# Optimization experiments

Measured on AMD Instinct MI355X. Metric: run time of the kernel, lower is better.

## Reference

```python
import jax, jax.numpy as jnp
import numpy as np

B, E, F, Q = 8, 2000, 6000, 20
D = 256   # entity_dim == word_dim (required: word_embedding output feeds LSTM with input_size=word_dim)
WD = 256
L = 3
NUM_ENTITY, NUM_REL, NUM_WORD = 400000, 6000, 60000
NNZ = 2 * B * F
PAGERANK_LAMBDA, FACT_SCALE = 0.8, 3.0
VERY_NEG = -100000000000.0
VERY_SMALL = 1e-10


def _lin(x, W, b):
    return x @ W.T + b


def _sparse_bmm(indices, values, x, num_rows):
    # indices: [3, nnz] = (batch, row, col); x: [B, C, Dx] -> out [B, num_rows, Dx]
    b, r, c = indices[0], indices[1], indices[2]
    contrib = values[:, None] * x[b, c]
    seg = b * num_rows + r
    out = jax.ops.segment_sum(contrib, seg, num_segments=x.shape[0] * num_rows)
    return out.reshape(x.shape[0], num_rows, x.shape[2])


def _lstm(x, Wih, Whh, bih, bhh):
    # PyTorch LSTM, batch_first, 1 layer, unidirectional; gate order i,f,g,o
    Bb, T, _ = x.shape
    H = Whh.shape[1]
    def step(carry, xt):
        h, c = carry
        g = xt @ Wih.T + bih + h @ Whh.T + bhh
        i, f, gg, o = jnp.split(g, 4, axis=-1)
        c = jax.nn.sigmoid(f) * c + jax.nn.sigmoid(i) * jnp.tanh(gg)
        h = jax.nn.sigmoid(o) * jnp.tanh(c)
        return (h, c), h
    init = (jnp.zeros((Bb, H), x.dtype), jnp.zeros((Bb, H), x.dtype))
    (h, c), hs = jax.lax.scan(step, init, jnp.swapaxes(x, 0, 1))
    return jnp.swapaxes(hs, 0, 1), h


def setup_inputs():
    key = jax.random.key(0)
    ks = iter(jax.random.split(key, 48))
    p = lambda shape: jax.random.normal(next(ks), shape, jnp.float32) * 0.02
    inp = {}
    inp['local_entity'] = jax.random.randint(next(ks), (B, E), 0, NUM_ENTITY + 1)
    inp['q2e_adj_mat'] = (jax.random.uniform(next(ks), (B, E, 1)) < 0.01).astype(jnp.float32)
    inp['kb_fact_rel'] = jax.random.randint(next(ks), (B, F), 0, NUM_REL)
    inp['query_text'] = jax.random.randint(next(ks), (B, Q), 0, NUM_WORD)
    inp['answer_dist'] = (jax.random.uniform(next(ks), (B, E)) < 0.005).astype(jnp.float32)
    eb = jax.random.randint(next(ks), (NNZ,), 0, B)
    ef = jax.random.randint(next(ks), (NNZ,), 0, F)
    ee = jax.random.randint(next(ks), (NNZ,), 0, E)
    inp['e2f_indices'] = jnp.stack([eb, ef, ee])
    inp['e2f_val'] = jnp.ones((NNZ,), jnp.float32)
    fb = jax.random.randint(next(ks), (NNZ,), 0, B)
    fe = jax.random.randint(next(ks), (NNZ,), 0, E)
    ff = jax.random.randint(next(ks), (NNZ,), 0, F)
    inp['f2e_indices'] = jnp.stack([fb, fe, ff])
    inp['f2e_val'] = jnp.ones((NNZ,), jnp.float32)
    inp['entity_table'] = p((NUM_ENTITY + 1, WD)).at[-1].set(0.0)
    inp['ent_lin_W'] = p((D, WD)); inp['ent_lin_b'] = jnp.zeros((D,), jnp.float32)
    inp['relation_table'] = p((NUM_REL + 1, WD)).at[-1].set(0.0)
    inp['rel_lin_W'] = p((D, WD)); inp['rel_lin_b'] = jnp.zeros((D,), jnp.float32)
    inp['word_table'] = p((NUM_WORD + 1, D)).at[-1].set(0.0)
    inp['lstm_Wih'] = p((4 * D, WD)); inp['lstm_Whh'] = p((4 * D, D))
    inp['lstm_bih'] = jnp.zeros((4 * D,), jnp.float32); inp['lstm_bhh'] = jnp.zeros((4 * D,), jnp.float32)
    inp['q2e_W'] = p((L, D, D)); inp['q2e_b'] = jnp.zeros((L, D), jnp.float32)
    inp['e2q_W'] = p((L, D, 3 * D)); inp['e2q_b'] = jnp.zeros((L, D), jnp.float32)
    inp['e2e_W'] = p((L, D, 3 * D)); inp['e2e_b'] = jnp.zeros((L, D), jnp.float32)
    inp['head_W'] = p((L, D, D)); inp['head_b'] = jnp.zeros((L, D), jnp.float32)
    inp['tail_W'] = p((L, D, D)); inp['tail_b'] = jnp.zeros((L, D), jnp.float32)
    inp['self_W'] = p((L, D, D)); inp['self_b'] = jnp.zeros((L, D), jnp.float32)
    inp['score_W'] = p((1, D)); inp['score_b'] = jnp.zeros((1,), jnp.float32)
    return inp


def reference(local_entity, q2e_adj_mat, kb_fact_rel, query_text, answer_dist, e2f_indices, e2f_val, f2e_indices, f2e_val, entity_table, ent_lin_W, ent_lin_b, relation_table, rel_lin_W, rel_lin_b, word_table, lstm_Wih, lstm_Whh, lstm_bih, lstm_bhh, q2e_W, q2e_b, e2q_W, e2q_b, e2e_W, e2e_b, head_W, head_b, tail_W, tail_b, self_W, self_b, score_W, score_b):
    query_mask = (query_text != NUM_WORD).astype(jnp.float32)          # [B,Q]
    local_entity_mask = (local_entity != NUM_ENTITY).astype(jnp.float32)
    # query encoder (dropout = identity in eval)
    query_hidden, h_last = _lstm(word_table[query_text], lstm_Wih, lstm_Whh, lstm_bih, lstm_bhh)
    query_node_emb = h_last[:, None, :]                                # [B,1,D]
    local_fact_emb = _lin(relation_table[kb_fact_rel], rel_lin_W, rel_lin_b)  # [B,F,D]
    div = jnp.sqrt(jnp.float32(D))
    sim = jnp.einsum('bqd,bfd->bqf', query_hidden, local_fact_emb) / div
    sim = jax.nn.softmax(sim + (1.0 - query_mask)[:, :, None] * VERY_NEG, axis=1)
    att = jnp.einsum('bqf,bqd->bfd', sim, query_hidden)
    Wt = jnp.sum(att * local_fact_emb, axis=2) / div                   # [B,F]
    W_tilde = jnp.exp(Wt - jnp.max(Wt, axis=1, keepdims=True))
    e2fT = jnp.stack([e2f_indices[0], e2f_indices[2], e2f_indices[1]])  # transpose(1,2)
    e2f_softmax = _sparse_bmm(e2fT, e2f_val, W_tilde[:, :, None], E)[..., 0]
    e2f_softmax = jnp.maximum(e2f_softmax, VERY_SMALL)
    pagerank_f = q2e_adj_mat[..., 0]                                    # [B,E]
    local_entity_emb = _lin(entity_table[local_entity], ent_lin_W, ent_lin_b)  # [B,E,D]
    for i in range(L):
        q2e_emb = jnp.broadcast_to(_lin(query_node_emb, q2e_W[i], q2e_b[i]), (B, E, D))
        nxt = jnp.concatenate([local_entity_emb, q2e_emb], axis=2)
        e2f_emb = jax.nn.relu(_lin(local_fact_emb, self_W[i], self_b[i]) + _sparse_bmm(e2f_indices, e2f_val, _lin(local_entity_emb, head_W[i], head_b[i]), F))
        e2f_norm = W_tilde[:, :, None] * _sparse_bmm(e2f_indices, e2f_val, (pagerank_f / e2f_softmax)[:, :, None], F)
        e2f_emb = e2f_emb * e2f_norm
        f2e_emb = jax.nn.relu(_lin(local_entity_emb, self_W[i], self_b[i]) + _sparse_bmm(f2e_indices, f2e_val, _lin(e2f_emb, tail_W[i], tail_b[i]), E))
        pagerank_f = PAGERANK_LAMBDA * _sparse_bmm(f2e_indices, f2e_val, e2f_norm, E)[..., 0] + (1.0 - PAGERANK_LAMBDA) * pagerank_f
        nxt = jnp.concatenate([nxt, FACT_SCALE * f2e_emb], axis=2)      # [B,E,3D]
        query_node_emb = jnp.einsum('be,bed->bd', pagerank_f, _lin(nxt, e2q_W[i], e2q_b[i]))[:, None, :]
        local_entity_emb = jax.nn.relu(_lin(nxt, e2e_W[i], e2e_b[i]))
    score = _lin(local_entity_emb, score_W, score_b)[..., 0]            # [B,E]
    loss = jnp.mean(jnp.maximum(score, 0.0) - score * answer_dist + jnp.log1p(jnp.exp(-jnp.abs(score))))
    score_m = score + (1.0 - local_entity_mask) * VERY_NEG
    pred = jnp.argmax(score_m, axis=1)
    pred_dist = jax.nn.sigmoid(score_m) * local_entity_mask
    return (loss, pred, pred_dist)
```

## Files before the change

### kernel.cpp

```cpp
#include <hip/hip_runtime.h>
#include <math.h>

#define BB 8
#define EE 2000
#define FF 6000
#define QQ 20
#define DD 256
#define NENT 400000
#define NWORD 60000
#define NNZ_ 96000
#define VNEG  (-1e11f)
#define VSMALL 1e-10f

typedef __attribute__((ext_vector_type(8))) short short8v;
typedef __attribute__((ext_vector_type(4))) short short4v;
typedef __attribute__((ext_vector_type(4))) float f32x4;

__device__ __forceinline__ unsigned short f2bf_rne(float x)
{
    unsigned u = __float_as_uint(x);
    u += 0x7FFFu + ((u >> 16) & 1u);
    return (unsigned short)(u >> 16);
}
__device__ __forceinline__ float bf2f(unsigned short h)
{
    return __uint_as_float((unsigned)h << 16);
}

template<int GATHER, int DUALW, int RELU, int RS, int BIASB>
__device__ __forceinline__ void mgemm_body(
    const float* __restrict__ A1, const int* __restrict__ idx,
    const float* __restrict__ A2, float sA2,
    const short* __restrict__ W1h, const short* __restrict__ W1l,
    const short* __restrict__ W2h, const short* __restrict__ W2l,
    const float* __restrict__ biasA,
    const float* __restrict__ rowscale, const float* __restrict__ bias2,
    float* __restrict__ out, int by, int bx,
    short* __restrict__ Ah, short* __restrict__ Al)
{
    const int tid = threadIdx.x;
    const int lane = tid & 63, wv = tid >> 6;
    const int wrow = wv >> 1, wcol = wv & 1;
    const int row0 = by * 128, col0 = bx * 128;

    const int sr = tid >> 1;
    const int sko = (tid & 1) << 5;
    const int grow = row0 + sr;
    const float* aRow1 = GATHER ? A1 + (size_t)idx[grow] * 256 : A1 + (size_t)grow * 256;
    const float* aRow2 = DUALW ? A2 + (size_t)grow * 256 : nullptr;

    f32x4 acc[4][4];
    #pragma unroll
    for (int i = 0; i < 4; ++i)
        #pragma unroll
        for (int j = 0; j < 4; ++j) acc[i][j] = (f32x4){0.f, 0.f, 0.f, 0.f};

    const int nch = DUALW ? 8 : 4;
    for (int ch = 0; ch < nch; ++ch) {
        const bool hi2 = DUALW && (ch >= 4);
        const float* ar = hi2 ? aRow2 : aRow1;
        const int kbase = (ch & 3) << 6;
        #pragma unroll
        for (int q = 0; q < 8; ++q) {
            const int kc = sko + (q << 2);
            float4 a = *(const float4*)(ar + kbase + kc);
            if (DUALW && hi2) { a.x *= sA2; a.y *= sA2; a.z *= sA2; a.w *= sA2; }
            unsigned short h0 = f2bf_rne(a.x), h1 = f2bf_rne(a.y),
                           h2 = f2bf_rne(a.z), h3 = f2bf_rne(a.w);
            unsigned short l0 = f2bf_rne(a.x - bf2f(h0)), l1 = f2bf_rne(a.y - bf2f(h1)),
                           l2 = f2bf_rne(a.z - bf2f(h2)), l3 = f2bf_rne(a.w - bf2f(h3));
            const int tI = ((sr >> 4) << 1) + (kc >> 5);
            const int off = (tI << 9) + ((((sr & 15)) + (((kc >> 3) & 3) << 4)) << 3) + (kc & 7);
            *(short4v*)(Ah + off) = (short4v){(short)h0, (short)h1, (short)h2, (short)h3};
            *(short4v*)(Al + off) = (short4v){(short)l0, (short)l1, (short)l2, (short)l3};
        }
        __syncthreads();
        const short* Wh = hi2 ? W2h : W1h;
        const short* Wl = hi2 ? W2l : W1l;
        #pragma unroll
        for (int ks = 0; ks < 2; ++ks) {
            const int kg = kbase + (ks << 5) + ((lane >> 4) << 3);
            short8v bh[4], bl[4];
            #pragma unroll
            for (int ct = 0; ct < 4; ++ct) {
                const int c = col0 + (wcol << 6) + (ct << 4) + (lane & 15);
                bh[ct] = *(const short8v*)(Wh + (size_t)c * 256 + kg);
                bl[ct] = *(const short8v*)(Wl + (size_t)c * 256 + kg);
            }
            #pragma unroll
            for (int rt = 0; rt < 4; ++rt) {
                const int tI = (((wrow << 2) + rt) << 1) + ks;
                const short8v avh = *(const short8v*)(Ah + (tI << 9) + (lane << 3));
                const short8v avl = *(const short8v*)(Al + (tI << 9) + (lane << 3));
                #pragma unroll
                for (int ct = 0; ct < 4; ++ct) {
                    acc[rt][ct] = __builtin_amdgcn_mfma_f32_16x16x32_bf16(avh, bh[ct], acc[rt][ct], 0, 0, 0);
                    acc[rt][ct] = __builtin_amdgcn_mfma_f32_16x16x32_bf16(avh, bl[ct], acc[rt][ct], 0, 0, 0);
                    acc[rt][ct] = __builtin_amdgcn_mfma_f32_16x16x32_bf16(avl, bh[ct], acc[rt][ct], 0, 0, 0);
                }
            }
        }
        __syncthreads();
    }
    #pragma unroll
    for (int rt = 0; rt < 4; ++rt) {
        const int rb = row0 + (wrow << 6) + (rt << 4) + ((lane >> 4) << 2);
        #pragma unroll
        for (int ct = 0; ct < 4; ++ct) {
            const int c = col0 + (wcol << 6) + (ct << 4) + (lane & 15);
            #pragma unroll
            for (int j = 0; j < 4; ++j) {
                const int r = rb + j;
                float v = acc[rt][ct][j];
                v += BIASB ? biasA[(size_t)(r / EE) * 256 + c] : biasA[c];
                if (RS) v += rowscale[r] * bias2[c];
                if (RELU) v = fmaxf(v, 0.f);
                out[(size_t)r * 256 + c] = v;
            }
        }
    }
}

template<int GATHER, int DUALW, int RELU, int RS, int BIASB>
__global__ __launch_bounds__(256, 2) void mgemm_k(
    const float* __restrict__ A1, const int* __restrict__ idx,
    const float* __restrict__ A2, float sA2,
    const short* __restrict__ W1h, const short* __restrict__ W1l,
    const short* __restrict__ W2h, const short* __restrict__ W2l,
    const float* __restrict__ biasA,
    const float* __restrict__ rowscale, const float* __restrict__ bias2,
    float* __restrict__ out)
{
    __shared__ short Ah[16 * 512];
    __shared__ short Al[16 * 512];
    mgemm_body<GATHER, DUALW, RELU, RS, BIASB>(A1, idx, A2, sA2, W1h, W1l, W2h, W2l,
        biasA, rowscale, bias2, out, blockIdx.y, blockIdx.x, Ah, Al);
}

template<int GATHER>
__global__ __launch_bounds__(256, 2) void mgemm_pair_k(
    const float* __restrict__ Aa, const int* __restrict__ idxA,
    const short* __restrict__ Wah, const short* __restrict__ Wal,
    const float* __restrict__ ba, float* __restrict__ outa, int nya,
    const float* __restrict__ Ab, const int* __restrict__ idxB,
    const short* __restrict__ Wbh, const short* __restrict__ Wbl,
    const float* __restrict__ bb, float* __restrict__ outb)
{
    __shared__ short Ah[16 * 512];
    __shared__ short Al[16 * 512];
    const int by = blockIdx.y;
    if (by < nya)
        mgemm_body<GATHER, 0, 0, 0, 0>(Aa, idxA, nullptr, 1.f, Wah, Wal, nullptr, nullptr,
            ba, nullptr, nullptr, outa, by, blockIdx.x, Ah, Al);
    else
        mgemm_body<GATHER, 0, 0, 0, 0>(Ab, idxB, nullptr, 1.f, Wbh, Wbl, nullptr, nullptr,
            bb, nullptr, nullptr, outb, by - nya, blockIdx.x, Ah, Al);
}

__global__ void wpack_k(const float* __restrict__ relW, const float* __restrict__ entW,
                        const float* __restrict__ headW, const float* __restrict__ tailW,
                        const float* __restrict__ selfW, const float* __restrict__ e2eW,
                        short* __restrict__ wh, short* __restrict__ wl)
{
    int id = blockIdx.x * 256 + threadIdx.x;
    if (id >= 17 * 65536) return;
    int m = id >> 16, e = id & 65535;
    float x;
    if (m == 0)       x = relW[e];
    else if (m == 1)  x = entW[e];
    else if (m < 5)   x = headW[(size_t)(m - 2) * 65536 + e];
    else if (m < 8)   x = tailW[(size_t)(m - 5) * 65536 + e];
    else if (m < 11)  x = selfW[(size_t)(m - 8) * 65536 + e];
    else if (m < 14)  x = e2eW[(size_t)(m - 11) * 196608 + (size_t)(e >> 8) * 768 + (e & 255)];
    else              x = e2eW[(size_t)(m - 14) * 196608 + (size_t)(e >> 8) * 768 + 512 + (e & 255)];
    unsigned short h = f2bf_rne(x);
    wh[id] = (short)h;
    wl[id] = (short)f2bf_rne(x - bf2f(h));
}

template<int GATHER>
__global__ __launch_bounds__(256, 4) void gemm3_k(
    const float* __restrict__ A1, const int* __restrict__ idx,
    const float* __restrict__ W1, int ldw1,
    const float* __restrict__ biasA,
    float* __restrict__ out, int M, int N)
{
    __shared__ float As[16][68];
    __shared__ float Bs[16][132];
    const int tid = threadIdx.x;
    const int row0 = blockIdx.y * 64, col0 = blockIdx.x * 128;
    const int tx = tid & 15, ty = tid >> 4;
    const int srA = tid >> 2, skA = (tid & 3) << 2;
    const int srB = tid >> 1, skB = (tid & 1) << 3;
    const int grA = row0 + srA;
    const bool rvalid = (grA < M);
    const float* aRow1 = nullptr;
    if (rvalid) aRow1 = GATHER ? A1 + (size_t)idx[grA] * 256 : A1 + (size_t)grA * 256;
    const float* wR1 = W1 + (size_t)(col0 + srB) * ldw1;

    float acc[4][8];
    #pragma unroll
    for (int i = 0; i < 4; ++i)
        #pragma unroll
        for (int j = 0; j < 8; ++j) acc[i][j] = 0.f;

    float4 a0, b0, b1;
    auto fetch = [&](int ch) {
        const int k0 = ch << 4;
        if (rvalid) a0 = *(const float4*)(aRow1 + k0 + skA);
        else        a0 = make_float4(0.f, 0.f, 0.f, 0.f);
        b0 = *(const float4*)(wR1 + k0 + skB);
        b1 = *(const float4*)(wR1 + k0 + skB + 4);
    };

    fetch(0);
    for (int ch = 0; ch < 16; ++ch) {
        As[skA + 0][srA] = a0.x; As[skA + 1][srA] = a0.y;
        As[skA + 2][srA] = a0.z; As[skA + 3][srA] = a0.w;
        Bs[skB + 0][srB] = b0.x; Bs[skB + 1][srB] = b0.y;
        Bs[skB + 2][srB] = b0.z; Bs[skB + 3][srB] = b0.w;
        Bs[skB + 4][srB] = b1.x; Bs[skB + 5][srB] = b1.y;
        Bs[skB + 6][srB] = b1.z; Bs[skB + 7][srB] = b1.w;
        __syncthreads();
        if (ch + 1 < 16) fetch(ch + 1);
        #pragma unroll
        for (int kk = 0; kk < 16; ++kk) {
            float av[4], bv[8];
            *(float4*)&av[0] = *(const float4*)&As[kk][ty << 2];
            *(float4*)&bv[0] = *(const float4*)&Bs[kk][tx << 2];
            *(float4*)&bv[4] = *(const float4*)&Bs[kk][(tx << 2) + 64];
            #pragma unroll
            for (int i = 0; i < 4; ++i)
                #pragma unroll
                for (int j = 0; j < 8; ++j) acc[i][j] += av[i] * bv[j];
        }
        __syncthreads();
    }
    #pragma unroll
    for (int i = 0; i < 4; ++i) {
        int r = row0 + (ty << 2) + i;
        if (r >= M) continue;
        float* orow = out + (size_t)r * N;
        #pragma unroll
        for (int jh = 0; jh < 2; ++jh) {
            const int c = col0 + (jh << 6) + (tx << 2);
            float4 v;
            v.x = acc[i][jh * 4 + 0] + biasA[c + 0];
            v.y = acc[i][jh * 4 + 1] + biasA[c + 1];
            v.z = acc[i][jh * 4 + 2] + biasA[c + 2];
            v.w = acc[i][jh * 4 + 3] + biasA[c + 3];
            *(float4*)(orow + c) = v;
        }
    }
}

__global__ void csr_count2_k(const int* __restrict__ idxA, int* __restrict__ cntA,
                             const int* __restrict__ idxB, int* __restrict__ cntB)
{
    int k = blockIdx.x * 256 + threadIdx.x;
    if (k >= NNZ_) return;
    if (blockIdx.y == 0) atomicAdd(&cntA[idxA[k] * FF + idxA[NNZ_ + k]], 1);
    else                 atomicAdd(&cntB[idxB[k] * EE + idxB[NNZ_ + k]], 1);
}

__global__ __launch_bounds__(1024) void scan2_k(
    const int* __restrict__ cntA, int* __restrict__ rpA, int* __restrict__ curA, int nA,
    const int* __restrict__ cntB, int* __restrict__ rpB, int* __restrict__ curB, int nB)
{
    const int* cnt = blockIdx.x ? cntB : cntA;
    int* rp  = blockIdx.x ? rpB  : rpA;
    int* cur = blockIdx.x ? curB : curA;
    int n    = blockIdx.x ? nB   : nA;
    __shared__ int sums[1024];
    int t = threadIdx.x;
    int chunk = (n + 1023) / 1024;
    int lo = t * chunk, hi = lo + chunk;
    if (lo > n) lo = n;
    if (hi > n) hi = n;
    int s = 0;
    for (int i = lo; i < hi; ++i) s += cnt[i];
    sums[t] = s;
    __syncthreads();
    for (int off = 1; off < 1024; off <<= 1) {
        int v = (t >= off) ? sums[t - off] : 0;
        __syncthreads();
        sums[t] += v;
        __syncthreads();
    }
    int run = (t == 0) ? 0 : sums[t - 1];
    for (int i = lo; i < hi; ++i) { rp[i] = run; cur[i] = run; run += cnt[i]; }
    if (hi == n) rp[n] = run;
}

__global__ void csr_fill2_k(
    const int* __restrict__ idxA, const float* __restrict__ valA,
    int* __restrict__ curA, int* __restrict__ colA, float* __restrict__ vpA,
    const int* __restrict__ idxB, const float* __restrict__ valB,
    int* __restrict__ curB, int* __restrict__ colB, float* __restrict__ vpB)
{
    int k = blockIdx.x * 256 + threadIdx.x;
    if (k >= NNZ_) return;
    if (blockIdx.y == 0) {
        int row = idxA[k] * FF + idxA[NNZ_ + k];
        int p = atomicAdd(&curA[row], 1);
        colA[p] = idxA[2 * NNZ_ + k];
        vpA[p] = valA[k];
    } else {
        int row = idxB[k] * EE + idxB[NNZ_ + k];
        int p = atomicAdd(&curB[row], 1);
        colB[p] = idxB[2 * NNZ_ + k];
        vpB[p] = valB[k];
    }
}

__global__ void degw_k(const int* __restrict__ rp, const float* __restrict__ vp,
                       float* __restrict__ degw, int n)
{
    int r = blockIdx.x * 256 + threadIdx.x;
    if (r >= n) return;
    float s = 0.f;
    for (int j = rp[r]; j < rp[r + 1]; ++j) s += vp[j];
    degw[r] = s;
}

__global__ __launch_bounds__(256) void gather_fused_e2f_k(
    const int* __restrict__ rowptr, const int* __restrict__ col,
    const float* __restrict__ valp, const float* __restrict__ headsrc,
    const float* __restrict__ pr, const float* __restrict__ sm,
    const float* __restrict__ Wtil, float* __restrict__ e2fnrm,
    float* __restrict__ dst, int nrows)
{
    int gid = blockIdx.x * 256 + threadIdx.x;
    int row = gid >> 6, lane = gid & 63;
    if (row >= nrows) return;
    int b = row / FF;
    const float* prb = pr + (size_t)b * EE;
    const float* smb = sm + (size_t)b * EE;
    float4* dp = (float4*)(dst + (size_t)row * DD + (lane << 2));
    float4 acc = *dp;
    float ns = 0.f;
    int j0 = rowptr[row], j1 = rowptr[row + 1];
    for (int j = j0; j < j1; ++j) {
        int c = col[j];
        float v = valp[j];
        float4 x = *(const float4*)(headsrc + ((size_t)b * EE + c) * DD + (lane << 2));
        acc.x += v * x.x; acc.y += v * x.y; acc.z += v * x.z; acc.w += v * x.w;
        ns += v * (prb[c] / fmaxf(smb[c], VSMALL));
    }
    float nrm = Wtil[row] * ns;
    if (lane == 0) e2fnrm[row] = nrm;
    acc.x = fmaxf(acc.x, 0.f) * nrm; acc.y = fmaxf(acc.y, 0.f) * nrm;
    acc.z = fmaxf(acc.z, 0.f) * nrm; acc.w = fmaxf(acc.w, 0.f) * nrm;
    *dp = acc;
}

__global__ __launch_bounds__(256) void gather_sum_k(
    const int* __restrict__ rowptr, const int* __restrict__ col,
    const float* __restrict__ valp, const float* __restrict__ src,
    float* __restrict__ dst, int nrows, int nrPerB, int ncs)
{
    int gid = blockIdx.x * 256 + threadIdx.x;
    int row = gid >> 6, lane = gid & 63;
    if (row >= nrows) return;
    int b = row / nrPerB;
    float4 acc = make_float4(0.f, 0.f, 0.f, 0.f);
    int j0 = rowptr[row], j1 = rowptr[row + 1];
    for (int j = j0; j < j1; ++j) {
        int c = col[j];
        float v = valp[j];
        float4 x = *(const float4*)(src + ((size_t)b * ncs + c) * DD + (lane << 2));
        acc.x += v * x.x; acc.y += v * x.y; acc.z += v * x.z; acc.w += v * x.w;
    }
    *(float4*)(dst + (size_t)row * DD + (lane << 2)) = acc;
}

#define LSTM_BLOCKS 64
__global__ __launch_bounds__(256, 1) void lstm2_k(
    const float* __restrict__ Xg, const float* __restrict__ Whh,
    const float* __restrict__ bhh, float* __restrict__ gbuf,
    unsigned* __restrict__ bar, float* __restrict__ qh, float* __restrict__ qne)
{
    __shared__ float wslice[128 * 257];
    __shared__ float hbuf[256];
    __shared__ float cbuf[256];
    __shared__ float gpart[256];
    const int B = blockIdx.x;
    const int b = B >> 3, p = B & 7;
    const int t = threadIdx.x;
    const float* wsrc = Whh + (size_t)p * 128 * 256;
    for (int i = t; i < 128 * 64; i += 256) {
        int row = i >> 6, q4 = (i & 63) << 2;
        float4 w = *(const float4*)(wsrc + (size_t)row * 256 + q4);
        float* d = &wslice[row * 257 + q4];
        d[0] = w.x; d[1] = w.y; d[2] = w.z; d[3] = w.w;
    }
    hbuf[t] = 0.f; cbuf[t] = 0.f;
    __syncthreads();

    unsigned* bar_cnt = bar;
    unsigned* bar_gen = bar + 1;

    for (int step = 0; step < QQ; ++step) {
        {
            const int r = t & 127, half = t >> 7;
            const float* wr = &wslice[r * 257 + half * 128];
            const float* hb = &hbuf[half * 128];
            float acc = 0.f;
            #pragma unroll 8
            for (int k = 0; k < 128; ++k) acc += wr[k] * hb[k];
            gpart[t] = acc;
        }
        __syncthreads();
        if (t < 128) {
            const int gr = p * 128 + t;
            float g = bhh[gr] + Xg[((size_t)b * QQ + step) * 1024 + gr]
                    + gpart[t] + gpart[t + 128];
            gbuf[((size_t)(step & 1) * BB + b) * 1024 + gr] = g;
        }
        __syncthreads();
        if (t == 0) {
            __threadfence();
            const unsigned target = (unsigned)(step + 1) * LSTM_BLOCKS;
            unsigned old = atomicAdd(bar_cnt, 1u);
            if (old == target - 1u) {
                atomicExch(bar_gen, (unsigned)(step + 1));
            } else {
                while (atomicAdd(bar_gen, 0u) < (unsigned)(step + 1)) {}
            }
            __threadfence();
        }
        __syncthreads();
        {
            const float* g = gbuf + ((size_t)(step & 1) * BB + b) * 1024;
            float gi = g[t], gf = g[256 + t], gg = g[512 + t], go = g[768 + t];
            float si = 1.f / (1.f + expf(-gi));
            float sf = 1.f / (1.f + expf(-gf));
            float so = 1.f / (1.f + expf(-go));
            float c = sf * cbuf[t] + si * tanhf(gg);
            float hh = so * tanhf(c);
            cbuf[t] = c;
            hbuf[t] = hh;
            if (p == 0) qh[((size_t)b * QQ + step) * DD + t] = hh;
        }
        __syncthreads();
    }
    if (p == 0) qne[(size_t)b * DD + t] = hbuf[t];
}

__global__ __launch_bounds__(256) void simwt_k(
    const float* __restrict__ qhid, const int* __restrict__ qtext,
    const float* __restrict__ lfe, float* __restrict__ Wt)
{
    __shared__ float qs[QQ * DD];
    __shared__ float qmn[QQ];
    const int b = blockIdx.y;
    const int f = blockIdx.x * 256 + threadIdx.x;
    for (int i = threadIdx.x; i < QQ * DD; i += 256) qs[i] = qhid[(size_t)b * QQ * DD + i];
    if (threadIdx.x < QQ)
        qmn[threadIdx.x] = (qtext[b * QQ + threadIdx.x] != NWORD) ? 0.f : VNEG;
    __syncthreads();
    if (f >= FF) return;
    float acc[QQ];
    #pragma unroll
    for (int q = 0; q < QQ; ++q) acc[q] = 0.f;
    const float* lr = lfe + ((size_t)b * FF + f) * DD;
    for (int d = 0; d < DD; d += 4) {
        float4 x = *(const float4*)(lr + d);
        #pragma unroll
        for (int q = 0; q < QQ; ++q) {
            float4 y = *(const float4*)&qs[q * DD + d];
            acc[q] += x.x * y.x + x.y * y.y + x.z * y.z + x.w * y.w;
        }
    }
    const float inv = 0.0625f;
    float pre[QQ], m = -INFINITY;
    #pragma unroll
    for (int q = 0; q < QQ; ++q) { pre[q] = acc[q] * inv + qmn[q]; m = fmaxf(m, pre[q]); }
    float s = 0.f;
    #pragma unroll
    for (int q = 0; q < QQ; ++q) s += expf(pre[q] - m);
    float wt = 0.f;
    #pragma unroll
    for (int q = 0; q < QQ; ++q) wt += (expf(pre[q] - m) / s) * (acc[q] * inv);
    Wt[(size_t)b * FF + f] = wt;
}

__global__ __launch_bounds__(256) void rowmax_wtil_k(
    const float* __restrict__ Wt, float* __restrict__ Wtil)
{
    __shared__ float red[256];
    int b = blockIdx.x, t = threadIdx.x;
    float m = -INFINITY;
    for (int f = t; f < FF; f += 256) m = fmaxf(m, Wt[b * FF + f]);
    red[t] = m; __syncthreads();
    for (int s = 128; s > 0; s >>= 1) {
        if (t < s) red[t] = fmaxf(red[t], red[t + s]);
        __syncthreads();
    }
    float mx = red[0];
    for (int f = t; f < FF; f += 256) Wtil[b * FF + f] = expf(Wt[b * FF + f] - mx);
}

__global__ void scatter_sm_k(const int* __restrict__ idx, const float* __restrict__ val,
                             const float* __restrict__ Wtil, float* __restrict__ dst)
{
    int k = blockIdx.x * 256 + threadIdx.x;
    if (k >= NNZ_) return;
    int b = idx[k], e = idx[2 * NNZ_ + k], f = idx[NNZ_ + k];
    atomicAdd(&dst[(size_t)b * EE + e], val[k] * Wtil[(size_t)b * FF + f]);
}

__global__ __launch_bounds__(256) void qlin_ebias_k(
    const float* __restrict__ qne, const float* __restrict__ q2eW,
    const float* __restrict__ q2eb, const float* __restrict__ e2eW,
    const float* __restrict__ e2eb, float* __restrict__ qlin, float* __restrict__ ebias)
{
    __shared__ float xs[DD], qs[DD];
    int b = blockIdx.x, j = threadIdx.x;
    xs[j] = qne[b * DD + j];
    __syncthreads();
    float acc = q2eb[j];
    const float* wr = q2eW + (size_t)j * DD;
    #pragma unroll 4
    for (int k = 0; k < DD; k += 4) {
        float4 w = *(const float4*)(wr + k);
        acc += xs[k] * w.x + xs[k + 1] * w.y + xs[k + 2] * w.z + xs[k + 3] * w.w;
    }
    qlin[b * DD + j] = acc;
    qs[j] = acc;
    __syncthreads();
    float acc2 = e2eb[j];
    const float* wr2 = e2eW + (size_t)j * 768 + 256;
    #pragma unroll 4
    for (int k = 0; k < DD; k += 4) {
        float4 w = *(const float4*)(wr2 + k);
        acc2 += qs[k] * w.x + qs[k + 1] * w.y + qs[k + 2] * w.z + qs[k + 3] * w.w;
    }
    ebias[b * DD + j] = acc2;
}

#define VCH 80
#define NCHK (EE / VCH)
__global__ __launch_bounds__(256) void vreduce_pr_k(
    const int* __restrict__ f2e_rp, const int* __restrict__ f2e_col,
    const float* __restrict__ f2e_vp, const float* __restrict__ e2fnrm,
    float* __restrict__ pr, const float* __restrict__ lee,
    const float* __restrict__ f2e, float* __restrict__ vpartL,
    float* __restrict__ vpartF, float* __restrict__ vpartS)
{
    int b = blockIdx.y, ch = blockIdx.x, k = threadIdx.x;
    int e0 = ch * VCH;
    __shared__ float prs[VCH];
    if (k < VCH) {
        int row = b * EE + e0 + k;
        float s = 0.f;
        for (int j = f2e_rp[row]; j < f2e_rp[row + 1]; ++j)
            s += f2e_vp[j] * e2fnrm[(size_t)b * FF + f2e_col[j]];
        float v = 0.8f * s + 0.2f * pr[row];
        pr[row] = v;
        prs[k] = v;
    }
    __syncthreads();
    float a1 = 0.f, a2 = 0.f;
    for (int e = 0; e < VCH; ++e) {
        float p = prs[e];
        size_t base = ((size_t)b * EE + e0 + e) * DD + k;
        a1 += p * lee[base];
        a2 += p * f2e[base];
    }
    int pi = ch * BB + b;
    vpartL[(size_t)pi * DD + k] = a1;
    vpartF[(size_t)pi * DD + k] = a2;
    float sp = 0.f;
    for (int e = k; e < VCH; e += 256) sp += prs[e];
    __shared__ float red[256];
    red[k] = sp; __syncthreads();
    for (int s = 128; s > 0; s >>= 1) {
        if (k < s) red[k] += red[k + s];
        __syncthreads();
    }
    if (k == 0) vpartS[pi] = red[0];
}

__global__ __launch_bounds__(256) void qneupd_qlin_k(
    const float* __restrict__ vpartL, const float* __restrict__ vpartF,
    const float* __restrict__ vpartS, const float* __restrict__ qlinCur,
    const float* __restrict__ W, const float* __restrict__ bias,
    float* __restrict__ qne,
    const float* __restrict__ q2eWn, const float* __restrict__ q2ebn,
    const float* __restrict__ e2eWn, const float* __restrict__ e2ebn,
    float* __restrict__ qlinNext, float* __restrict__ ebiasNext)
{
    __shared__ float s1[DD], s2[DD], s3[DD], qn[DD], qs[DD];
    int b = blockIdx.x, j = threadIdx.x;
    float a1 = 0.f, a3 = 0.f, sp = 0.f;
    for (int ch = 0; ch < NCHK; ++ch) {
        int pi = ch * BB + b;
        a1 += vpartL[(size_t)pi * DD + j];
        a3 += vpartF[(size_t)pi * DD + j];
        sp += vpartS[pi];
    }
    s1[j] = a1; s2[j] = qlinCur[b * DD + j]; s3[j] = a3;
    __syncthreads();
    float acc = sp * bias[j];
    const float* wr = W + (size_t)j * 768;
    #pragma unroll 4
    for (int k = 0; k < DD; k += 4) {
        float4 w0 = *(const float4*)(wr + k);
        float4 w1 = *(const float4*)(wr + 256 + k);
        float4 w2 = *(const float4*)(wr + 512 + k);
        acc += s1[k] * w0.x + s1[k + 1] * w0.y + s1[k + 2] * w0.z + s1[k + 3] * w0.w;
        acc += sp * (s2[k] * w1.x + s2[k + 1] * w1.y + s2[k + 2] * w1.z + s2[k + 3] * w1.w);
        acc += 3.f * (s3[k] * w2.x + s3[k + 1] * w2.y + s3[k + 2] * w2.z + s3[k + 3] * w2.w);
    }
    qne[b * DD + j] = acc;
    qn[j] = acc;
    __syncthreads();
    float aq = q2ebn[j];
    const float* wq = q2eWn + (size_t)j * DD;
    #pragma unroll 4
    for (int k = 0; k < DD; k += 4) {
        float4 w = *(const float4*)(wq + k);
        aq += qn[k] * w.x + qn[k + 1] * w.y + qn[k + 2] * w.z + qn[k + 3] * w.w;
    }
    qlinNext[b * DD + j] = aq;
    qs[j] = aq;
    __syncthreads();
    float ae = e2ebn[j];
    const float* we = e2eWn + (size_t)j * 768 + 256;
    #pragma unroll 4
    for (int k = 0; k < DD; k += 4) {
        float4 w = *(const float4*)(we + k);
        ae += qs[k] * w.x + qs[k + 1] * w.y + qs[k + 2] * w.z + qs[k + 3] * w.w;
    }
    ebiasNext[b * DD + j] = ae;
}

__global__ __launch_bounds__(256) void final_part_k(
    const float* __restrict__ lee, const float* __restrict__ sw_,
    const float* __restrict__ sb, const int* __restrict__ local_entity,
    const float* __restrict__ ans, float* __restrict__ out,
    float* __restrict__ fpl, float* __restrict__ fpv, int* __restrict__ fpi)
{
    __shared__ float sw[DD];
    int b = blockIdx.x >> 3, ch = blockIdx.x & 7, t = threadIdx.x;
    sw[t] = sw_[t];
    __syncthreads();
    float sb0 = sb[0];
    float lsum = 0.f, bm = -INFINITY;
    int bi = EE;
    int e0 = ch * 250;
    for (int e = e0 + t; e < e0 + 250; e += 256) {
        const float* a = lee + ((size_t)b * EE + e) * DD;
        float s = sb0;
        for (int k = 0; k < DD; k += 4) {
            float4 v = *(const float4*)(a + k);
            s += v.x * sw[k] + v.y * sw[k + 1] + v.z * sw[k + 2] + v.w * sw[k + 3];
        }
        float mask = (local_entity[b * EE + e] != NENT) ? 1.f : 0.f;
        float smv = s + (1.f - mask) * VNEG;
        float sig;
        if (smv >= 0.f) sig = 1.f / (1.f + expf(-smv));
        else { float es = expf(smv); sig = es / (1.f + es); }
        out[1 + BB + b * EE + e] = sig * mask;
        lsum += fmaxf(s, 0.f) - s * ans[b * EE + e] + log1pf(expf(-fabsf(s)));
        if (smv > bm) { bm = smv; bi = e; }
    }
    __shared__ float rv[256]; __shared__ int ri[256]; __shared__ float rl[256];
    rv[t] = bm; ri[t] = bi; rl[t] = lsum;
    __syncthreads();
    for (int s = 128; s > 0; s >>= 1) {
        if (t < s) {
            rl[t] += rl[t + s];
            if (rv[t + s] > rv[t] || (rv[t + s] == rv[t] && ri[t + s] < ri[t])) {
                rv[t] = rv[t + s]; ri[t] = ri[t + s];
            }
        }
        __syncthreads();
    }
    if (t == 0) { fpl[blockIdx.x] = rl[0]; fpv[blockIdx.x] = rv[0]; fpi[blockIdx.x] = ri[0]; }
}

__global__ void final_combine_k(const float* __restrict__ fpl,
                                const float* __restrict__ fpv,
                                const int* __restrict__ fpi, float* __restrict__ out)
{
    __shared__ float lsums[BB];
    int t = threadIdx.x;
    if (t < BB) {
        float ls = 0.f, bm = -INFINITY;
        int bi = EE;
        for (int ch = 0; ch < 8; ++ch) {
            int i = t * 8 + ch;
            ls += fpl[i];
            if (fpv[i] > bm || (fpv[i] == bm && fpi[i] < bi)) { bm = fpv[i]; bi = fpi[i]; }
        }
        out[1 + t] = (float)bi;
        lsums[t] = ls;
    }
    __syncthreads();
    if (t == 0) {
        float s = 0.f;
        for (int b = 0; b < BB; ++b) s += lsums[b];
        out[0] = s / (float)(BB * EE);
    }
}

extern "C" void kernel_launch(void* const* d_in, const int* in_sizes, int n_in,
                              void* d_out, int out_size, void* d_ws, size_t ws_size,
                              hipStream_t stream)
{
    (void)in_sizes; (void)n_in; (void)out_size; (void)ws_size;
    const int*   local_entity = (const int*)d_in[0];
    const float* q2e_adj      = (const float*)d_in[1];
    const int*   kb_fact_rel  = (const int*)d_in[2];
    const int*   query_text   = (const int*)d_in[3];
    const float* answer_dist  = (const float*)d_in[4];
    const int*   e2f_idx      = (const int*)d_in[5];
    const float* e2f_val      = (const float*)d_in[6];
    const int*   f2e_idx      = (const int*)d_in[7];
    const float* f2e_val      = (const float*)d_in[8];
    const float* entity_table = (const float*)d_in[9];
    const float* ent_W        = (const float*)d_in[10];
    const float* ent_b        = (const float*)d_in[11];
    const float* rel_table    = (const float*)d_in[12];
    const float* rel_W        = (const float*)d_in[13];
    const float* rel_b        = (const float*)d_in[14];
    const float* word_table   = (const float*)d_in[15];
    const float* Wih          = (const float*)d_in[16];
    const float* Whh          = (const float*)d_in[17];
    const float* bih          = (const float*)d_in[18];
    const float* bhh          = (const float*)d_in[19];
    const float* q2e_W        = (const float*)d_in[20];
    const float* q2e_b        = (const float*)d_in[21];
    const float* e2q_W        = (const float*)d_in[22];
    const float* e2q_b        = (const float*)d_in[23];
    const float* e2e_W        = (const float*)d_in[24];
    const float* e2e_b        = (const float*)d_in[25];
    const float* head_W       = (const float*)d_in[26];
    const float* head_b       = (const float*)d_in[27];
    const float* tail_W       = (const float*)d_in[28];
    const float* tail_b       = (const float*)d_in[29];
    const float* self_W       = (const float*)d_in[30];
    const float* self_b       = (const float*)d_in[31];
    const float* score_W      = (const float*)d_in[32];
    const float* score_b      = (const float*)d_in[33];

    const int NR1 = BB * FF;
    const int NR2 = BB * EE;

    float* ws = (float*)d_ws;
    size_t off = 0;
    auto alloc = [&](size_t n) { float* p = ws + off; off += n; return p; };
    auto salloc = [&](size_t nshorts) { short* p = (short*)(ws + off); off += (nshorts + 1) / 2; return p; };
    float* Xg      = alloc((size_t)BB * QQ * 1024);
    float* gbuf    = alloc((size_t)2 * BB * 1024);
    float* qh      = alloc((size_t)BB * QQ * DD);
    float* qne     = alloc(BB * DD);
    float* lfe     = alloc((size_t)NR1 * DD);
    float* leeA    = alloc((size_t)NR2 * DD);
    float* leeB    = alloc((size_t)NR2 * DD);
    float* Wt      = alloc(BB * FF);
    float* Wtil    = alloc(BB * FF);
    float* e2fsm   = alloc(BB * EE);
    float* pr      = alloc(BB * EE);
    float* qlinA   = alloc(BB * DD);
    float* qlinB   = alloc(BB * DD);
    float* ebiasA  = alloc(BB * DD);
    float* ebiasB  = alloc(BB * DD);
    float* e2fnrm  = alloc(BB * FF);
    float* fpl     = alloc(64);
    float* fpv     = alloc(64);
    float* bufC    = alloc((size_t)NR2 * DD);
    float* e2fT    = alloc((size_t)NR1 * DD);
    float* f2eT    = alloc((size_t)NR2 * DD);
    float* tmp     = alloc((size_t)NR2 * DD);
    float* vpartL  = alloc((size_t)NCHK * BB * DD);
    float* vpartF  = alloc((size_t)NCHK * BB * DD);
    float* vpartS  = alloc(NCHK * BB);
    float* degw2   = alloc(NR2);
    float* e2f_vp  = alloc(NNZ_);
    float* f2e_vp  = alloc(NNZ_);
    short* wbh     = salloc((size_t)17 * 65536);
    short* wbl     = salloc((size_t)17 * 65536);
    int* ib = (int*)(ws + off);
    size_t ioff = 0;
    auto ialloc = [&](size_t n) { int* p = ib + ioff; ioff += n; return p; };
    int* e2f_cnt = ialloc(NR1);
    int* e2f_rp  = ialloc(NR1 + 1);
    int* e2f_cur = ialloc(NR1);
    int* e2f_col = ialloc(NNZ_);
    int* f2e_cnt = ialloc(NR2);
    int* f2e_rp  = ialloc(NR2 + 1);
    int* f2e_cur = ialloc(NR2);
    int* f2e_col = ialloc(NNZ_);
    int* fpi     = ialloc(64);
    unsigned* bar = (unsigned*)ialloc(2);

    auto WH = [&](int m) { return wbh + (size_t)m * 65536; };
    auto WL = [&](int m) { return wbl + (size_t)m * 65536; };

    float* outp = (float*)d_out;
    const int SCB = (NNZ_ + 255) / 256;

    wpack_k<<<(17 * 65536) / 256, 256, 0, stream>>>(rel_W, ent_W, head_W, tail_W,
                                                    self_W, e2e_W, wbh, wbl);

    hipMemsetAsync(e2f_cnt, 0, NR1 * sizeof(int), stream);
    hipMemsetAsync(f2e_cnt, 0, NR2 * sizeof(int), stream);
    csr_count2_k<<<dim3(SCB, 2), 256, 0, stream>>>(e2f_idx, e2f_cnt, f2e_idx, f2e_cnt);
    scan2_k<<<2, 1024, 0, stream>>>(e2f_cnt, e2f_rp, e2f_cur, NR1,
                                    f2e_cnt, f2e_rp, f2e_cur, NR2);
    csr_fill2_k<<<dim3(SCB, 2), 256, 0, stream>>>(
        e2f_idx, e2f_val, e2f_cur, e2f_col, e2f_vp,
        f2e_idx, f2e_val, f2e_cur, f2e_col, f2e_vp);
    degw_k<<<(NR2 + 255) / 256, 256, 0, stream>>>(f2e_rp, f2e_vp, degw2, NR2);

    gemm3_k<1><<<dim3(8, 3), 256, 0, stream>>>(
        word_table, query_text, Wih, 256, bih, Xg, BB * QQ, 1024);
    hipMemsetAsync(bar, 0, 2 * sizeof(unsigned), stream);
    lstm2_k<<<LSTM_BLOCKS, 256, 0, stream>>>(Xg, Whh, bhh, gbuf, bar, qh, qne);

    mgemm_pair_k<1><<<dim3(2, 375 + 125), 256, 0, stream>>>(
        rel_table, kb_fact_rel, WH(0), WL(0), rel_b, lfe, 375,
        entity_table, local_entity, WH(1), WL(1), ent_b, leeA);

    simwt_k<<<dim3((FF + 255) / 256, BB), 256, 0, stream>>>(qh, query_text, lfe, Wt);
    rowmax_wtil_k<<<BB, 256, 0, stream>>>(Wt, Wtil);

    hipMemsetAsync(e2fsm, 0, BB * EE * sizeof(float), stream);
    scatter_sm_k<<<SCB, 256, 0, stream>>>(e2f_idx, e2f_val, Wtil, e2fsm);

    hipMemcpyAsync(pr, q2e_adj, BB * EE * sizeof(float), hipMemcpyDeviceToDevice, stream);
    qlin_ebias_k<<<BB, 256, 0, stream>>>(qne, q2e_W, q2e_b, e2e_W, e2e_b, qlinA, ebiasA);

    float* lee = leeA;   float* lee2 = leeB;
    float* qlinCur = qlinA;  float* qlinNxt = qlinB;
    float* ebiasCur = ebiasA; float* ebiasNxt = ebiasB;

    for (int i = 0; i < 3; ++i) {
        const float* headbi = head_b + i * DD;
        const float* tailbi = tail_b + i * DD;
        const float* selfbi = self_b + i * DD;

        mgemm_pair_k<0><<<dim3(2, 125 + 375), 256, 0, stream>>>(
            lee, nullptr, WH(2 + i), WL(2 + i), headbi, bufC, 125,
            lfe, nullptr, WH(8 + i), WL(8 + i), selfbi, e2fT);

        gather_fused_e2f_k<<<(NR1 * 64) / 256, 256, 0, stream>>>(
            e2f_rp, e2f_col, e2f_vp, bufC, pr, e2fsm, Wtil, e2fnrm, e2fT, NR1);

        gather_sum_k<<<(NR2 * 64) / 256, 256, 0, stream>>>(
            f2e_rp, f2e_col, f2e_vp, e2fT, tmp, NR2, EE, FF);

        mgemm_k<0, 1, 1, 1, 0><<<dim3(2, 125), 256, 0, stream>>>(
            lee, nullptr, tmp, 1.f, WH(8 + i), WL(8 + i), WH(5 + i), WL(5 + i),
            selfbi, degw2, tailbi, f2eT);

        if (i < 2) {
            vreduce_pr_k<<<dim3(NCHK, BB), 256, 0, stream>>>(
                f2e_rp, f2e_col, f2e_vp, e2fnrm, pr, lee, f2eT, vpartL, vpartF, vpartS);
            const float* e2qWi = e2q_W + (size_t)i * DD * 3 * DD;
            const float* e2qbi = e2q_b + i * DD;
            const float* q2eWn = q2e_W + (size_t)(i + 1) * DD * DD;
            const float* q2ebn = q2e_b + (i + 1) * DD;
            const float* e2eWn = e2e_W + (size_t)(i + 1) * DD * 3 * DD;
            const float* e2ebn = e2e_b + (i + 1) * DD;
            qneupd_qlin_k<<<BB, 256, 0, stream>>>(
                vpartL, vpartF, vpartS, qlinCur, e2qWi, e2qbi, qne,
                q2eWn, q2ebn, e2eWn, e2ebn, qlinNxt, ebiasNxt);
        }

        mgemm_k<0, 1, 1, 0, 1><<<dim3(2, 125), 256, 0, stream>>>(
            lee, nullptr, f2eT, 3.f, WH(11 + i), WL(11 + i), WH(14 + i), WL(14 + i),
            ebiasCur, nullptr, nullptr, lee2);

        { float* t = lee; lee = lee2; lee2 = t; }
        if (i < 2) {
            { float* t = qlinCur; qlinCur = qlinNxt; qlinNxt = t; }
            { float* t = ebiasCur; ebiasCur = ebiasNxt; ebiasNxt = t; }
        }
    }

    final_part_k<<<64, 256, 0, stream>>>(lee, score_W, score_b, local_entity,
                                         answer_dist, outp, fpl, fpv, fpi);
    final_combine_k<<<1, 64, 0, stream>>>(fpl, fpv, fpi, outp);
}
```

Baseline: 1.124 ms.

## Merge prologue kernels and co-launch vreduce with e2e GEMM

Weight packing, CSR counting and the query-embedding input GEMM are combined into one prologue kernel that dispatches on block index. In the layer loop, the pagerank/vector-reduce blocks now run in the same grid as the e2e GEMM blocks through a new tail kernel. The aim is to cut launch count and let small, independent workloads fill the GPU at the same time. The cost is extra LDS use and a __launch_bounds__(256,2) limit on the fused tail kernel. The fused kernel is also launched before qneupd_qlin, which only works because the e2e GEMM uses the current ebias.

```diff
diff --git a/kernel.cpp b/kernel.cpp
--- a/kernel.cpp
+++ b/kernel.cpp
@@ -157,45 +157,90 @@
             bb, nullptr, nullptr, outb, by - nya, blockIdx.x, Ah, Al);
 }
 
-__global__ void wpack_k(const float* __restrict__ relW, const float* __restrict__ entW,
-                        const float* __restrict__ headW, const float* __restrict__ tailW,
-                        const float* __restrict__ selfW, const float* __restrict__ e2eW,
-                        short* __restrict__ wh, short* __restrict__ wl)
-{
-    int id = blockIdx.x * 256 + threadIdx.x;
-    if (id >= 17 * 65536) return;
-    int m = id >> 16, e = id & 65535;
-    float x;
-    if (m == 0)       x = relW[e];
-    else if (m == 1)  x = entW[e];
-    else if (m < 5)   x = headW[(size_t)(m - 2) * 65536 + e];
-    else if (m < 8)   x = tailW[(size_t)(m - 5) * 65536 + e];
-    else if (m < 11)  x = selfW[(size_t)(m - 8) * 65536 + e];
-    else if (m < 14)  x = e2eW[(size_t)(m - 11) * 196608 + (size_t)(e >> 8) * 768 + (e & 255)];
-    else              x = e2eW[(size_t)(m - 14) * 196608 + (size_t)(e >> 8) * 768 + 512 + (e & 255)];
-    unsigned short h = f2bf_rne(x);
-    wh[id] = (short)h;
-    wl[id] = (short)f2bf_rne(x - bf2f(h));
-}
-
-template<int GATHER>
-__global__ __launch_bounds__(256, 4) void gemm3_k(
+#define VCH 80
+#define NCHK (EE / VCH)
+__device__ __forceinline__ void vreduce_body(
+    int ch, int b, int k,
+    const int* __restrict__ f2e_rp, const int* __restrict__ f2e_col,
+    const float* __restrict__ f2e_vp, const float* __restrict__ e2fnrm,
+    float* __restrict__ pr, const float* __restrict__ lee,
+    const float* __restrict__ f2e, float* __restrict__ vpartL,
+    float* __restrict__ vpartF, float* __restrict__ vpartS,
+    float* __restrict__ lds)
+{
+    float* prs = lds;
+    float* red = lds + 128;
+    int e0 = ch * VCH;
+    if (k < VCH) {
+        int row = b * EE + e0 + k;
+        float s = 0.f;
+        for (int j = f2e_rp[row]; j < f2e_rp[row + 1]; ++j)
+            s += f2e_vp[j] * e2fnrm[(size_t)b * FF + f2e_col[j]];
+        float v = 0.8f * s + 0.2f * pr[row];
+        pr[row] = v;
+        prs[k] = v;
+    }
+    __syncthreads();
+    float a1 = 0.f, a2 = 0.f;
+    for (int e = 0; e < VCH; ++e) {
+        float p = prs[e];
+        size_t base = ((size_t)b * EE + e0 + e) * DD + k;
+        a1 += p * lee[base];
+        a2 += p * f2e[base];
+    }
+    int pi = ch * BB + b;
+    vpartL[(size_t)pi * DD + k] = a1;
+    vpartF[(size_t)pi * DD + k] = a2;
+    float sp = 0.f;
+    for (int e = k; e < VCH; e += 256) sp += prs[e];
+    red[k] = sp; __syncthreads();
+    for (int s = 128; s > 0; s >>= 1) {
+        if (k < s) red[k] += red[k + s];
+        __syncthreads();
+    }
+    if (k == 0) vpartS[pi] = red[0];
+}
+
+template<int DOV>
+__global__ __launch_bounds__(256, 2) void tail_k(
+    const float* __restrict__ lee, const float* __restrict__ f2eT,
+    const short* __restrict__ WaH, const short* __restrict__ WaL,
+    const short* __restrict__ WbH, const short* __restrict__ WbL,
+    const float* __restrict__ ebias, float* __restrict__ lee2,
+    const int* __restrict__ f2e_rp, const int* __restrict__ f2e_col,
+    const float* __restrict__ f2e_vp, const float* __restrict__ e2fnrm,
+    float* __restrict__ pr, float* __restrict__ vpartL,
+    float* __restrict__ vpartF, float* __restrict__ vpartS)
+{
+    __shared__ char ldsbuf[32768];
+    int blk = blockIdx.x;
+    if (blk < 250) {
+        short* Ah = (short*)ldsbuf; short* Al = Ah + 8192;
+        mgemm_body<0, 1, 1, 0, 1>(lee, nullptr, f2eT, 3.f, WaH, WaL, WbH, WbL,
+            ebias, nullptr, nullptr, lee2, blk >> 1, blk & 1, Ah, Al);
+    } else if (DOV) {
+        int v = blk - 250;
+        vreduce_body(v >> 3, v & 7, threadIdx.x, f2e_rp, f2e_col, f2e_vp, e2fnrm,
+                     pr, lee, f2eT, vpartL, vpartF, vpartS, (float*)ldsbuf);
+    }
+}
+
+__device__ __forceinline__ void gemm3_body(
     const float* __restrict__ A1, const int* __restrict__ idx,
     const float* __restrict__ W1, int ldw1,
     const float* __restrict__ biasA,
-    float* __restrict__ out, int M, int N)
-{
-    __shared__ float As[16][68];
-    __shared__ float Bs[16][132];
+    float* __restrict__ out, int M, int N, int by, int bx,
+    float (*As)[68], float (*Bs)[132])
+{
     const int tid = threadIdx.x;
-    const int row0 = blockIdx.y * 64, col0 = blockIdx.x * 128;
+    const int row0 = by * 64, col0 = bx * 128;
     const int tx = tid & 15, ty = tid >> 4;
     const int srA = tid >> 2, skA = (tid & 3) << 2;
     const int srB = tid >> 1, skB = (tid & 1) << 3;
     const int grA = row0 + srA;
     const bool rvalid = (grA < M);
     const float* aRow1 = nullptr;
-    if (rvalid) aRow1 = GATHER ? A1 + (size_t)idx[grA] * 256 : A1 + (size_t)grA * 256;
+    if (rvalid) aRow1 = A1 + (size_t)idx[grA] * 256;
     const float* wR1 = W1 + (size_t)(col0 + srB) * ldw1;
 
     float acc[4][8];
@@ -254,13 +299,45 @@
     }
 }
 
-__global__ void csr_count2_k(const int* __restrict__ idxA, int* __restrict__ cntA,
-                             const int* __restrict__ idxB, int* __restrict__ cntB)
-{
-    int k = blockIdx.x * 256 + threadIdx.x;
-    if (k >= NNZ_) return;
-    if (blockIdx.y == 0) atomicAdd(&cntA[idxA[k] * FF + idxA[NNZ_ + k]], 1);
-    else                 atomicAdd(&cntB[idxB[k] * EE + idxB[NNZ_ + k]], 1);
+__global__ __launch_bounds__(256, 4) void prologue_k(
+    const float* __restrict__ relW, const float* __restrict__ entW,
+    const float* __restrict__ headW, const float* __restrict__ tailW,
+    const float* __restrict__ selfW, const float* __restrict__ e2eW,
+    short* __restrict__ wh, short* __restrict__ wl,
+    const int* __restrict__ e2f_idx, int* __restrict__ e2f_cnt,
+    const int* __restrict__ f2e_idx, int* __restrict__ f2e_cnt,
+    const float* __restrict__ word_table, const int* __restrict__ query_text,
+    const float* __restrict__ Wih, const float* __restrict__ bih,
+    float* __restrict__ Xg)
+{
+    __shared__ char lds[12800];
+    int blk = blockIdx.x;
+    if (blk < 4352) {
+        int id = blk * 256 + threadIdx.x;
+        int m = id >> 16, e = id & 65535;
+        float x;
+        if (m == 0)       x = relW[e];
+        else if (m == 1)  x = entW[e];
+        else if (m < 5)   x = headW[(size_t)(m - 2) * 65536 + e];
+        else if (m < 8)   x = tailW[(size_t)(m - 5) * 65536 + e];
+        else if (m < 11)  x = selfW[(size_t)(m - 8) * 65536 + e];
+        else if (m < 14)  x = e2eW[(size_t)(m - 11) * 196608 + (size_t)(e >> 8) * 768 + (e & 255)];
+        else              x = e2eW[(size_t)(m - 14) * 196608 + (size_t)(e >> 8) * 768 + 512 + (e & 255)];
+        unsigned short h = f2bf_rne(x);
+        wh[id] = (short)h;
+        wl[id] = (short)f2bf_rne(x - bf2f(h));
+    } else if (blk < 5102) {
+        int c = blk - 4352;
+        int k = (c % 375) * 256 + threadIdx.x;
+        if (c < 375) atomicAdd(&e2f_cnt[e2f_idx[k] * FF + e2f_idx[NNZ_ + k]], 1);
+        else         atomicAdd(&f2e_cnt[f2e_idx[k] * EE + f2e_idx[NNZ_ + k]], 1);
+    } else {
+        int g = blk - 5102;
+        float (*As)[68]  = (float(*)[68])lds;
+        float (*Bs)[132] = (float(*)[132])(lds + 4352);
+        gemm3_body(word_table, query_text, Wih, 256, bih, Xg,
+                   BB * QQ, 1024, g / 8, g % 8, As, Bs);
+    }
 }
 
 __global__ __launch_bounds__(1024) void scan2_k(
@@ -537,49 +614,6 @@
         acc2 += qs[k] * w.x + qs[k + 1] * w.y + qs[k + 2] * w.z + qs[k + 3] * w.w;
     }
     ebias[b * DD + j] = acc2;
-}
-
-#define VCH 80
-#define NCHK (EE / VCH)
-__global__ __launch_bounds__(256) void vreduce_pr_k(
-    const int* __restrict__ f2e_rp, const int* __restrict__ f2e_col,
-    const float* __restrict__ f2e_vp, const float* __restrict__ e2fnrm,
-    float* __restrict__ pr, const float* __restrict__ lee,
-    const float* __restrict__ f2e, float* __restrict__ vpartL,
-    float* __restrict__ vpartF, float* __restrict__ vpartS)
-{
-    int b = blockIdx.y, ch = blockIdx.x, k = threadIdx.x;
-    int e0 = ch * VCH;
-    __shared__ float prs[VCH];
-    if (k < VCH) {
-        int row = b * EE + e0 + k;
-        float s = 0.f;
-        for (int j = f2e_rp[row]; j < f2e_rp[row + 1]; ++j)
-            s += f2e_vp[j] * e2fnrm[(size_t)b * FF + f2e_col[j]];
-        float v = 0.8f * s + 0.2f * pr[row];
-        pr[row] = v;
-        prs[k] = v;
-    }
-    __syncthreads();
-    float a1 = 0.f, a2 = 0.f;
-    for (int e = 0; e < VCH; ++e) {
-        float p = prs[e];
-        size_t base = ((size_t)b * EE + e0 + e) * DD + k;
-        a1 += p * lee[base];
-        a2 += p * f2e[base];
-    }
-    int pi = ch * BB + b;
-    vpartL[(size_t)pi * DD + k] = a1;
-    vpartF[(size_t)pi * DD + k] = a2;
-    float sp = 0.f;
-    for (int e = k; e < VCH; e += 256) sp += prs[e];
-    __shared__ float red[256];
-    red[k] = sp; __syncthreads();
-    for (int s = 128; s > 0; s >>= 1) {
-        if (k < s) red[k] += red[k + s];
-        __syncthreads();
-    }
-    if (k == 0) vpartS[pi] = red[0];
 }
 
 __global__ __launch_bounds__(256) void qneupd_qlin_k(
@@ -803,12 +837,14 @@
     float* outp = (float*)d_out;
     const int SCB = (NNZ_ + 255) / 256;
 
-    wpack_k<<<(17 * 65536) / 256, 256, 0, stream>>>(rel_W, ent_W, head_W, tail_W,
-                                                    self_W, e2e_W, wbh, wbl);
-
     hipMemsetAsync(e2f_cnt, 0, NR1 * sizeof(int), stream);
     hipMemsetAsync(f2e_cnt, 0, NR2 * sizeof(int), stream);
-    csr_count2_k<<<dim3(SCB, 2), 256, 0, stream>>>(e2f_idx, e2f_cnt, f2e_idx, f2e_cnt);
+    hipMemsetAsync(bar, 0, 2 * sizeof(unsigned), stream);
+    prologue_k<<<5126, 256, 0, stream>>>(
+        rel_W, ent_W, head_W, tail_W, self_W, e2e_W, wbh, wbl,
+        e2f_idx, e2f_cnt, f2e_idx, f2e_cnt,
+        word_table, query_text, Wih, bih, Xg);
+
     scan2_k<<<2, 1024, 0, stream>>>(e2f_cnt, e2f_rp, e2f_cur, NR1,
                                     f2e_cnt, f2e_rp, f2e_cur, NR2);
     csr_fill2_k<<<dim3(SCB, 2), 256, 0, stream>>>(
@@ -816,9 +852,6 @@
         f2e_idx, f2e_val, f2e_cur, f2e_col, f2e_vp);
     degw_k<<<(NR2 + 255) / 256, 256, 0, stream>>>(f2e_rp, f2e_vp, degw2, NR2);
 
-    gemm3_k<1><<<dim3(8, 3), 256, 0, stream>>>(
-        word_table, query_text, Wih, 256, bih, Xg, BB * QQ, 1024);
-    hipMemsetAsync(bar, 0, 2 * sizeof(unsigned), stream);
     lstm2_k<<<LSTM_BLOCKS, 256, 0, stream>>>(Xg, Whh, bhh, gbuf, bar, qh, qne);
 
     mgemm_pair_k<1><<<dim3(2, 375 + 125), 256, 0, stream>>>(
@@ -858,8 +891,10 @@
             selfbi, degw2, tailbi, f2eT);
 
         if (i < 2) {
-            vreduce_pr_k<<<dim3(NCHK, BB), 256, 0, stream>>>(
-                f2e_rp, f2e_col, f2e_vp, e2fnrm, pr, lee, f2eT, vpartL, vpartF, vpartS);
+            tail_k<1><<<450, 256, 0, stream>>>(
+                lee, f2eT, WH(11 + i), WL(11 + i), WH(14 + i), WL(14 + i),
+                ebiasCur, lee2,
+                f2e_rp, f2e_col, f2e_vp, e2fnrm, pr, vpartL, vpartF, vpartS);
             const float* e2qWi = e2q_W + (size_t)i * DD * 3 * DD;
             const float* e2qbi = e2q_b + i * DD;
             const float* q2eWn = q2e_W + (size_t)(i + 1) * DD * DD;
@@ -869,11 +904,12 @@
             qneupd_qlin_k<<<BB, 256, 0, stream>>>(
                 vpartL, vpartF, vpartS, qlinCur, e2qWi, e2qbi, qne,
                 q2eWn, q2ebn, e2eWn, e2ebn, qlinNxt, ebiasNxt);
-        }
-
-        mgemm_k<0, 1, 1, 0, 1><<<dim3(2, 125), 256, 0, stream>>>(
-            lee, nullptr, f2eT, 3.f, WH(11 + i), WL(11 + i), WH(14 + i), WL(14 + i),
-            ebiasCur, nullptr, nullptr, lee2);
+        } else {
+            tail_k<0><<<250, 256, 0, stream>>>(
+                lee, f2eT, WH(11 + i), WL(11 + i), WH(14 + i), WL(14 + i),
+                ebiasCur, lee2,
+                f2e_rp, f2e_col, f2e_vp, e2fnrm, pr, vpartL, vpartF, vpartS);
+        }
 
         { float* t = lee; lee = lee2; lee2 = t; }
         if (i < 2) {
```

Result: no change. 1.103 ms (-1.9%).
